# Kernel optimization log

Hardware: AMD Instinct MI355X
Metric: run time of the kernel (lower is better)

The kernel has to match this reference:

```python
import jax, jax.numpy as jnp
import numpy as np

TOPK = 300
NUM_LEVELS = 3
GATE_TEMP = 1.0


def _normalized_grid(h, w):
    # matches torch: linspace(-1,1) meshgrid 'ij', stack (xx, yy) -> [h*w, 2]
    y = jnp.linspace(-1.0, 1.0, h, dtype=jnp.float32)
    x = jnp.linspace(-1.0, 1.0, w, dtype=jnp.float32)
    yy, xx = jnp.meshgrid(y, x, indexing='ij')
    return jnp.stack((xx, yy), axis=-1).reshape(h * w, 2)


def setup_inputs() -> dict:
    key = jax.random.key(0)
    ks = jax.random.split(key, 10)
    C, H_DIM, MAXL = 256, 256, 8
    shapes = [(8, C, 100, 152), (8, C, 50, 76), (8, C, 25, 38)]
    inp = {}
    for i, s in enumerate(shapes):
        inp[f'f{i}'] = jax.random.normal(ks[i], s, dtype=jnp.float32)
    inp['conv_w'] = jax.random.normal(ks[3], (C,), dtype=jnp.float32) * (1.0 / np.sqrt(C))
    inp['conv_b'] = jnp.zeros((1,), dtype=jnp.float32)
    inp['level_emb'] = jax.random.normal(ks[4], (MAXL, H_DIM), dtype=jnp.float32)
    qin = C + H_DIM + 3  # 515
    inp['w1'] = jax.random.normal(ks[5], (qin, H_DIM), dtype=jnp.float32) * (1.0 / np.sqrt(qin))
    inp['b1'] = jnp.zeros((H_DIM,), dtype=jnp.float32)
    inp['w2'] = jax.random.normal(ks[6], (H_DIM, H_DIM), dtype=jnp.float32) * (1.0 / np.sqrt(H_DIM))
    inp['b2'] = jnp.zeros((H_DIM,), dtype=jnp.float32)
    inp['gate_w'] = jax.random.normal(ks[7], (H_DIM, MAXL), dtype=jnp.float32) * (1.0 / np.sqrt(H_DIM))
    inp['gate_b'] = jnp.zeros((MAXL,), dtype=jnp.float32)
    inp['residual_scale'] = jnp.zeros((1,), dtype=jnp.float32)  # residual_scale_init=0.0
    return inp


def reference(f0, f1, f2, conv_w, conv_b, level_emb, w1, b1, w2, b2, gate_w, gate_b, residual_scale):
    levels = [f0, f1, f2]
    B = f0.shape[0]
    tok_s, tok_f, tok_p, tok_l = [], [], [], []
    for i, f in enumerate(levels):
        _, C, H, W = f.shape
        # 1x1 conv proxy objectness score -> [B, H*W]
        s = jnp.einsum('bchw,c->bhw', f, conv_w).reshape(B, H * W) + conv_b[0]
        tok_s.append(s)
        tok_f.append(f.reshape(B, C, H * W).transpose(0, 2, 1))       # [B, HW, C]
        tok_p.append(jnp.broadcast_to(_normalized_grid(H, W), (B, H * W, 2)))
        tok_l.append(jnp.full((B, H * W), i, dtype=jnp.int32))
    scores = jnp.concatenate(tok_s, axis=1)   # [B, N]
    feats = jnp.concatenate(tok_f, axis=1)    # [B, N, C]
    pos = jnp.concatenate(tok_p, axis=1)      # [B, N, 2]
    lvl = jnp.concatenate(tok_l, axis=1)      # [B, N]

    top_vals, top_idx = jax.lax.top_k(scores, TOPK)                     # [B, K]
    fk = jnp.take_along_axis(feats, top_idx[:, :, None], axis=1)        # [B, K, C]
    pk = jnp.take_along_axis(pos, top_idx[:, :, None], axis=1)          # [B, K, 2]
    lk = jnp.take_along_axis(lvl, top_idx, axis=1)                      # [B, K]
    sp = jax.nn.sigmoid(top_vals)                                       # [B, K]

    q = jnp.concatenate([fk, level_emb[lk], pk, sp[..., None]], axis=-1)  # [B, K, C+H+3]
    h = jax.nn.relu(q @ w1 + b1)
    h = jax.nn.relu(h @ w2 + b2)
    logits = (h @ gate_w + gate_b)[..., :NUM_LEVELS]                     # [B, K, L]
    gates = jax.nn.softmax(logits / GATE_TEMP, axis=-1)
    alpha = gates.mean(axis=1)                                           # [B, L]
    scale = 1.0 + residual_scale[0] * alpha                              # [B, L]

    outs = [f * scale[:, i][:, None, None, None] for i, f in enumerate(levels)]
    # flatten the output feature dict into one [B, sum(C*H*W)] array
    return jnp.concatenate([o.reshape(B, -1) for o in outs], axis=1)
```

## Files before the change

kernel.cpp:

```cpp
#include <hip/hip_runtime.h>
#include <hip/hip_bf16.h>

#define NTOK 19950
#define NTOKP 19968
#define KTOP 300
#define NB 8
#define NQ 2400
#define QDIM 520
#define NCC 16

typedef float f32x4 __attribute__((ext_vector_type(4)));

__device__ __forceinline__ uint32_t fkey(float f) {
    uint32_t u = __float_as_uint(f);
    return (u & 0x80000000u) ? ~u : (u | 0x80000000u);
}

__global__ __launch_bounds__(256) void score_part_kernel(
    const float* __restrict__ f0, const float* __restrict__ f1, const float* __restrict__ f2,
    const float* __restrict__ conv_w, float* __restrict__ partial, int* __restrict__ ghist)
{
    __shared__ float cwch[16];
    const int tid = threadIdx.x;
    const int blk = blockIdx.x;
    int b, cc;
    if (blk < 512)      { b = blk >> 6; cc = (blk >> 2) & 15; }
    else if (blk < 640) { int i = blk - 512; b = i >> 4; cc = i & 15; }
    else                { int i = blk - 640; b = i >> 4; cc = i & 15; }
    if (blk >= 640 && ((blk - 640) & 15) == 0 && tid < 256)
        ghist[((blk - 640) >> 4) * 256 + tid] = 0;
    if (tid < 16) cwch[tid] = conv_w[cc * 16 + tid];
    __syncthreads();

    if (blk < 512) {
        const int q = blk & 3;
        const f32x4* b4 = (const f32x4*)(f0 + ((size_t)(b * 256 + cc * 16)) * 15200) + q * 950;
        const int s3 = (tid + 768 < 950) ? tid + 768 : 0;
        f32x4 a0 = {0,0,0,0}, a1 = a0, a2 = a0, a3 = a0;
        #pragma unroll 4
        for (int c = 0; c < 16; ++c) {
            const f32x4* r = b4 + (size_t)c * 3800;
            const float w = cwch[c];
            f32x4 v0 = r[tid], v1 = r[tid + 256], v2 = r[tid + 512], v3 = r[s3];
            a0 += v0 * w; a1 += v1 * w; a2 += v2 * w; a3 += v3 * w;
        }
        f32x4* o4 = (f32x4*)(partial + (size_t)(cc * NB + b) * NTOKP) + q * 950;
        o4[tid] = a0; o4[tid + 256] = a1; o4[tid + 512] = a2;
        if (tid + 768 < 950) o4[tid + 768] = a3;
    } else if (blk < 640) {
        const f32x4* b4 = (const f32x4*)(f1 + ((size_t)(b * 256 + cc * 16)) * 3800);
        const int s3 = (tid + 768 < 950) ? tid + 768 : 0;
        f32x4 a0 = {0,0,0,0}, a1 = a0, a2 = a0, a3 = a0;
        #pragma unroll 4
        for (int c = 0; c < 16; ++c) {
            const f32x4* r = b4 + (size_t)c * 950;
            const float w = cwch[c];
            f32x4 v0 = r[tid], v1 = r[tid + 256], v2 = r[tid + 512], v3 = r[s3];
            a0 += v0 * w; a1 += v1 * w; a2 += v2 * w; a3 += v3 * w;
        }
        f32x4* o4 = (f32x4*)(partial + (size_t)(cc * NB + b) * NTOKP + 15200);
        o4[tid] = a0; o4[tid + 256] = a1; o4[tid + 512] = a2;
        if (tid + 768 < 950) o4[tid + 768] = a3;
    } else {
        const float2* b2 = (const float2*)(f2 + ((size_t)(b * 256 + cc * 16)) * 950);
        const int s1 = (tid + 256 < 475) ? tid + 256 : 0;
        float2 a0 = {0,0}, a1 = a0;
        #pragma unroll 4
        for (int c = 0; c < 16; ++c) {
            const float2* r = b2 + (size_t)c * 475;
            const float w = cwch[c];
            float2 v0 = r[tid], v1 = r[s1];
            a0.x += v0.x * w; a0.y += v0.y * w;
            a1.x += v1.x * w; a1.y += v1.y * w;
        }
        float2* o2 = (float2*)(partial + (size_t)(cc * NB + b) * NTOKP + 19000);
        o2[tid] = a0;
        if (tid + 256 < 475) o2[tid + 256] = a1;
    }
}

__global__ __launch_bounds__(256) void score_reduce_kernel(
    const float* __restrict__ partial, const float* __restrict__ conv_b,
    float* __restrict__ scores, int* __restrict__ ghist)
{
    __shared__ int lh[256];
    const int tid = threadIdx.x;
    const int b = blockIdx.y;
    const int i = blockIdx.x * 256 + tid;
    lh[tid] = 0;
    __syncthreads();
    if (i < NTOK) {
        float s = 0.0f;
        #pragma unroll
        for (int cc = 0; cc < NCC; ++cc)
            s += partial[(size_t)(cc * NB + b) * NTOKP + i];
        s += conv_b[0];
        scores[b * NTOK + i] = s;
        atomicAdd(&lh[fkey(s) >> 24], 1);
    }
    __syncthreads();
    if (lh[tid]) atomicAdd(&ghist[b * 256 + tid], lh[tid]);
}

__global__ __launch_bounds__(1024, 1) void topk_kernel(
    const float* __restrict__ scores, const int* __restrict__ ghist,
    int* __restrict__ top_idx)
{
    __shared__ uint32_t key[NTOK];
    __shared__ int whist[16][256];
    __shared__ int suffix[257];
    __shared__ uint32_t s_prefix;
    __shared__ int s_Kr, s_cnt, s_tcnt;
    __shared__ int tie[1024];
    const int tid = threadIdx.x;
    const int wv = tid >> 6;
    const int b = blockIdx.x;
    const float* srow = scores + b * NTOK;
    for (int i = tid; i < NTOK; i += 1024) key[i] = fkey(srow[i]);
    if (tid == 0) { s_Kr = KTOP; suffix[256] = 0; }
    if (tid < 256) suffix[tid] = ghist[b * 256 + tid];
    __syncthreads();
    if (tid < 64) {
        const int c0 = suffix[tid * 4], c1 = suffix[tid * 4 + 1];
        const int c2 = suffix[tid * 4 + 2], c3 = suffix[tid * 4 + 3];
        const int tot = c0 + c1 + c2 + c3;
        int s = tot;
        #pragma unroll
        for (int off = 1; off < 64; off <<= 1) {
            int o = __shfl_down(s, off);
            if (tid + off < 64) s += o;
        }
        const int Sn = s - tot;
        suffix[tid * 4 + 3] = c3 + Sn;
        suffix[tid * 4 + 2] = c2 + c3 + Sn;
        suffix[tid * 4 + 1] = c1 + c2 + c3 + Sn;
        suffix[tid * 4 + 0] = tot + Sn;
    }
    __syncthreads();
    if (tid < 256) {
        int sgeq = suffix[tid];
        int sgt  = suffix[tid + 1];
        if (sgeq >= KTOP && sgt < KTOP) {
            s_prefix = (uint32_t)tid << 24;
            s_Kr = KTOP - sgt;
        }
    }
    __syncthreads();
    uint32_t pmask = 0xFF000000u;
    for (int pass = 1; pass < 4; ++pass) {
        const int shift = 24 - 8 * pass;
        for (int i = tid; i < 16 * 256; i += 1024) ((int*)whist)[i] = 0;
        __syncthreads();
        const uint32_t prefix = s_prefix;
        const int Kr = s_Kr;
        for (int i = tid; i < NTOK; i += 1024) {
            uint32_t k = key[i];
            if ((k & pmask) == prefix) atomicAdd(&whist[wv][(k >> shift) & 255], 1);
        }
        __syncthreads();
        if (tid < 256) {
            int s = 0;
            #pragma unroll
            for (int w = 0; w < 16; ++w) s += whist[w][tid];
            suffix[tid] = s;
        }
        __syncthreads();
        if (tid < 64) {
            const int c0 = suffix[tid * 4], c1 = suffix[tid * 4 + 1];
            const int c2 = suffix[tid * 4 + 2], c3 = suffix[tid * 4 + 3];
            const int tot = c0 + c1 + c2 + c3;
            int s = tot;
            #pragma unroll
            for (int off = 1; off < 64; off <<= 1) {
                int o = __shfl_down(s, off);
                if (tid + off < 64) s += o;
            }
            const int Sn = s - tot;
            suffix[tid * 4 + 3] = c3 + Sn;
            suffix[tid * 4 + 2] = c2 + c3 + Sn;
            suffix[tid * 4 + 1] = c1 + c2 + c3 + Sn;
            suffix[tid * 4 + 0] = tot + Sn;
        }
        __syncthreads();
        if (tid < 256) {
            int sgeq = suffix[tid];
            int sgt  = suffix[tid + 1];
            if (sgeq >= Kr && sgt < Kr) {
                s_prefix = prefix | ((uint32_t)tid << shift);
                s_Kr = Kr - sgt;
            }
        }
        __syncthreads();
        pmask |= (0xFFu << shift);
    }
    const uint32_t T = s_prefix;
    const int need = s_Kr;
    if (tid == 0) { s_cnt = 0; s_tcnt = 0; }
    __syncthreads();
    for (int i = tid; i < NTOK; i += 1024) {
        uint32_t k = key[i];
        if (k > T) {
            int p = atomicAdd(&s_cnt, 1);
            top_idx[b * KTOP + p] = i;
        } else if (k == T) {
            int p = atomicAdd(&s_tcnt, 1);
            if (p < 1024) tie[p] = i;
        }
    }
    __syncthreads();
    if (tid == 0) {
        int base = s_cnt;
        int tcnt = s_tcnt > 1024 ? 1024 : s_tcnt;
        for (int s = 0; s < need; ++s) {
            int mi = s;
            for (int u = s + 1; u < tcnt; ++u) if (tie[u] < tie[mi]) mi = u;
            int tmp = tie[s]; tie[s] = tie[mi]; tie[mi] = tmp;
            top_idx[b * KTOP + base + s] = tie[s];
        }
    }
}

#define QT 8
__global__ __launch_bounds__(512, 1) void mlp_kernel(
    const float* __restrict__ f0, const float* __restrict__ f1, const float* __restrict__ f2,
    const float* __restrict__ scores, const int* __restrict__ top_idx,
    const float* __restrict__ level_emb,
    const float* __restrict__ w1, const float* __restrict__ b1,
    const float* __restrict__ w2, const float* __restrict__ b2,
    const float* __restrict__ gate_w, const float* __restrict__ gate_b,
    float* __restrict__ G)
{
    __shared__ __align__(16) float q[QT][QDIM];
    __shared__ __align__(16) float part[QT][256];
    __shared__ __align__(16) float h[QT][256];
    __shared__ int s_b[QT], s_lvl[QT], s_hw[QT], s_HW[QT];
    const int tid = threadIdx.x;
    const int out = tid & 255;
    const int kh = tid >> 8;
    const int k0 = blockIdx.x * QT;

    if (tid < QT) {
        const int kk = k0 + tid;
        const int bq = kk / KTOP;
        const int idx = top_idx[kk];
        int lvl, hw, HWl, Wl, Hl;
        if (idx < 15200)      { lvl = 0; hw = idx;         HWl = 15200; Wl = 152; Hl = 100; }
        else if (idx < 19000) { lvl = 1; hw = idx - 15200; HWl = 3800;  Wl = 76;  Hl = 50;  }
        else                  { lvl = 2; hw = idx - 19000; HWl = 950;   Wl = 38;  Hl = 25;  }
        s_b[tid] = bq; s_lvl[tid] = lvl; s_hw[tid] = hw; s_HW[tid] = HWl;
        int hh = hw / Wl, ww = hw - hh * Wl;
        float x = -1.0f + 2.0f * (float)ww / (float)(Wl - 1);
        float y = -1.0f + 2.0f * (float)hh / (float)(Hl - 1);
        float sv = scores[bq * NTOK + idx];
        float sp = 1.0f / (1.0f + expf(-sv));
        q[tid][512] = x; q[tid][513] = y; q[tid][514] = sp;
        q[tid][515] = 0.0f; q[tid][516] = 0.0f; q[tid][517] = 0.0f;
        q[tid][518] = 0.0f; q[tid][519] = 0.0f;
    }
    __syncthreads();
    #pragma unroll
    for (int j = tid; j < QT * 256; j += 512) {
        const int t = j >> 8, c = j & 255;
        const int lvl = s_lvl[t];
        const float* f = (lvl == 0) ? f0 : ((lvl == 1) ? f1 : f2);
        q[t][c]       = f[((size_t)(s_b[t] * 256 + c)) * s_HW[t] + s_hw[t]];
        q[t][256 + c] = level_emb[lvl * 256 + c];
    }
    __syncthreads();

    float acc[QT];

    {
        #pragma unroll
        for (int t = 0; t < QT; ++t) acc[t] = 0.0f;
        const float* wp = w1 + (size_t)(kh * 256) * 256 + out;
        float a0 = wp[0], a1 = wp[256], a2 = wp[512], a3 = wp[768];
        for (int i4 = 0; i4 < 64; ++i4) {
            float c0 = a0, c1 = a1, c2 = a2, c3 = a3;
            const float* wn = wp + 1024;
            if (i4 < 63) { a0 = wn[0]; a1 = wn[256]; a2 = wn[512]; a3 = wn[768]; }
            wp = wn;
            const int kb = kh * 256 + i4 * 4;
            #pragma unroll
            for (int t = 0; t < QT; ++t) {
                float4 qv = *reinterpret_cast<const float4*>(&q[t][kb]);
                acc[t] += qv.x * c0 + qv.y * c1 + qv.z * c2 + qv.w * c3;
            }
        }
        if (kh) {
            for (int r = 512; r < 515; ++r) {
                float wv = w1[(size_t)r * 256 + out];
                #pragma unroll
                for (int t = 0; t < QT; ++t) acc[t] += q[t][r] * wv;
            }
            #pragma unroll
            for (int t = 0; t < QT; ++t) part[t][out] = acc[t];
        }
    }
    __syncthreads();
    if (kh == 0) {
        float bj = b1[out];
        #pragma unroll
        for (int t = 0; t < QT; ++t) h[t][out] = fmaxf(acc[t] + part[t][out] + bj, 0.0f);
    }
    __syncthreads();

    {
        #pragma unroll
        for (int t = 0; t < QT; ++t) acc[t] = 0.0f;
        const float* wp = w2 + (size_t)(kh * 128) * 256 + out;
        float a0 = wp[0], a1 = wp[256], a2 = wp[512], a3 = wp[768];
        for (int i4 = 0; i4 < 32; ++i4) {
            float c0 = a0, c1 = a1, c2 = a2, c3 = a3;
            const float* wn = wp + 1024;
            if (i4 < 31) { a0 = wn[0]; a1 = wn[256]; a2 = wn[512]; a3 = wn[768]; }
            wp = wn;
            const int kb = kh * 128 + i4 * 4;
            #pragma unroll
            for (int t = 0; t < QT; ++t) {
                float4 hv = *reinterpret_cast<const float4*>(&h[t][kb]);
                acc[t] += hv.x * c0 + hv.y * c1 + hv.z * c2 + hv.w * c3;
            }
        }
        if (kh) {
            #pragma unroll
            for (int t = 0; t < QT; ++t) part[t][out] = acc[t];
        }
    }
    __syncthreads();
    if (kh == 0) {
        float bj = b2[out];
        #pragma unroll
        for (int t = 0; t < QT; ++t) q[t][out] = fmaxf(acc[t] + part[t][out] + bj, 0.0f);
    }
    __syncthreads();

    if (tid < 256) {
        const int t = tid >> 5, seg = tid & 31;
        float l0 = 0.f, l1 = 0.f, l2 = 0.f;
        for (int c = seg * 8; c < seg * 8 + 8; ++c) {
            float hv = q[t][c];
            l0 += hv * gate_w[c * 8 + 0];
            l1 += hv * gate_w[c * 8 + 1];
            l2 += hv * gate_w[c * 8 + 2];
        }
        float* gp = &part[0][0];
        gp[(t * 32 + seg) * 3 + 0] = l0;
        gp[(t * 32 + seg) * 3 + 1] = l1;
        gp[(t * 32 + seg) * 3 + 2] = l2;
    }
    __syncthreads();
    if (tid < QT) {
        const int t = tid;
        float l0 = gate_b[0], l1 = gate_b[1], l2 = gate_b[2];
        const float* gp = &part[0][0];
        for (int seg = 0; seg < 32; ++seg) {
            l0 += gp[(t * 32 + seg) * 3 + 0];
            l1 += gp[(t * 32 + seg) * 3 + 1];
            l2 += gp[(t * 32 + seg) * 3 + 2];
        }
        float m = fmaxf(l0, fmaxf(l1, l2));
        float e0 = expf(l0 - m), e1 = expf(l1 - m), e2 = expf(l2 - m);
        float inv = 1.0f / (e0 + e1 + e2);
        G[(k0 + t) * 3 + 0] = e0 * inv;
        G[(k0 + t) * 3 + 1] = e1 * inv;
        G[(k0 + t) * 3 + 2] = e2 * inv;
    }
}

__global__ __launch_bounds__(256) void out_kernel(
    const f32x4* __restrict__ f0, const f32x4* __restrict__ f1, const f32x4* __restrict__ f2,
    const float* __restrict__ G, const float* __restrict__ rs, f32x4* __restrict__ out)
{
    __shared__ float red[3][32];
    __shared__ float ssc[3];
    const int b = blockIdx.y;
    const int tid = threadIdx.x;
    if (tid < 96) {
        const int l = tid / 32, c = tid % 32;
        float s = 0.0f;
        const int kb = c * 10;
        const int ke = (kb + 10 < KTOP) ? kb + 10 : KTOP;
        for (int k = kb; k < ke; ++k) s += G[(size_t)(b * KTOP + k) * 3 + l];
        red[l][c] = s;
    }
    __syncthreads();
    for (int off = 16; off > 0; off >>= 1) {
        if (tid < 96) {
            const int l = tid / 32, c = tid % 32;
            if (c < off) red[l][c] += red[l][c + off];
        }
        __syncthreads();
    }
    if (tid < 3) ssc[tid] = 1.0f + rs[0] * (red[tid][0] / (float)KTOP);
    __syncthreads();

    const int t0 = blockIdx.x * 256 + tid;
    const int TPB = gridDim.x * 256;
    f32x4* ob = out + (size_t)b * 1276800;
    {
        const float sc = ssc[0];
        const f32x4* src = f0 + (size_t)b * 972800;
        for (int r = t0; r < 972800; r += TPB)
            __builtin_nontemporal_store(src[r] * sc, &ob[r]);
    }
    {
        const float sc = ssc[1];
        const f32x4* src = f1 + (size_t)b * 243200;
        f32x4* o1 = ob + 972800;
        for (int r = t0; r < 243200; r += TPB)
            __builtin_nontemporal_store(src[r] * sc, &o1[r]);
    }
    {
        const float sc = ssc[2];
        const f32x4* src = f2 + (size_t)b * 60800;
        f32x4* o2 = ob + 1216000;
        for (int r = t0; r < 60800; r += TPB)
            __builtin_nontemporal_store(src[r] * sc, &o2[r]);
    }
}

extern "C" void kernel_launch(void* const* d_in, const int* in_sizes, int n_in,
                              void* d_out, int out_size, void* d_ws, size_t ws_size,
                              hipStream_t stream)
{
    const float* f0        = (const float*)d_in[0];
    const float* f1        = (const float*)d_in[1];
    const float* f2        = (const float*)d_in[2];
    const float* conv_w    = (const float*)d_in[3];
    const float* conv_b    = (const float*)d_in[4];
    const float* level_emb = (const float*)d_in[5];
    const float* w1        = (const float*)d_in[6];
    const float* b1        = (const float*)d_in[7];
    const float* w2        = (const float*)d_in[8];
    const float* b2        = (const float*)d_in[9];
    const float* gate_w    = (const float*)d_in[10];
    const float* gate_b    = (const float*)d_in[11];
    const float* rs        = (const float*)d_in[12];

    char* ws = (char*)d_ws;
    float* scores  = (float*)ws;
    int*   top_idx = (int*)(ws + 640 * 1024);
    float* G       = (float*)(ws + 656 * 1024);
    int*   ghist   = (int*)(ws + 688 * 1024);
    float* partial = (float*)(ws + 704 * 1024);

    score_part_kernel<<<768, 256, 0, stream>>>(f0, f1, f2, conv_w, partial, ghist);
    score_reduce_kernel<<<dim3(78, NB), 256, 0, stream>>>(partial, conv_b, scores, ghist);
    topk_kernel<<<NB, 1024, 0, stream>>>(scores, ghist, top_idx);
    mlp_kernel<<<NQ / QT, 512, 0, stream>>>(f0, f1, f2, scores, top_idx, level_emb,
                                            w1, b1, w2, b2, gate_w, gate_b, G);
    out_kernel<<<dim3(256, NB), 256, 0, stream>>>((const f32x4*)f0, (const f32x4*)f1,
                                                  (const f32x4*)f2, G, rs, (f32x4*)d_out);
}
```

Before: 150.2 us.

## Compact top-k candidates to top-byte bucket and widen output kernel grid

The top-k kernel no longer stores all 19950 keys in shared memory. It emits elements whose top byte lies above the threshold bucket directly and compacts the threshold-bucket elements into a small candidate buffer, so the three refinement passes scan only those candidates. It falls back to rescanning global scores when more than 4096 candidates land in the bucket. The per-wave histograms become a single shared histogram, which means more atomic contention but much less shared memory. The out_kernel grid is doubled from 256 to 512 blocks per batch, and a store guard is added in the score kernel.

```diff
diff --git a/kernel.cpp b/kernel.cpp
--- a/kernel.cpp
+++ b/kernel.cpp
@@ -8,12 +8,32 @@
 #define NQ 2400
 #define QDIM 520
 #define NCC 16
+#define CAND 4096
 
 typedef float f32x4 __attribute__((ext_vector_type(4)));
 
 __device__ __forceinline__ uint32_t fkey(float f) {
     uint32_t u = __float_as_uint(f);
     return (u & 0x80000000u) ? ~u : (u | 0x80000000u);
+}
+
+__device__ __forceinline__ void suffix_scan_256(int* hist, int tid) {
+    if (tid < 64) {
+        const int c0 = hist[tid * 4], c1 = hist[tid * 4 + 1];
+        const int c2 = hist[tid * 4 + 2], c3 = hist[tid * 4 + 3];
+        const int tot = c0 + c1 + c2 + c3;
+        int s = tot;
+        #pragma unroll
+        for (int off = 1; off < 64; off <<= 1) {
+            int o = __shfl_down(s, off);
+            if (tid + off < 64) s += o;
+        }
+        const int Sn = s - tot;
+        hist[tid * 4 + 3] = c3 + Sn;
+        hist[tid * 4 + 2] = c2 + c3 + Sn;
+        hist[tid * 4 + 1] = c1 + c2 + c3 + Sn;
+        hist[tid * 4 + 0] = tot + Sn;
+    }
 }
 
 __global__ __launch_bounds__(256) void score_part_kernel(
@@ -74,7 +94,7 @@
             a1.x += v1.x * w; a1.y += v1.y * w;
         }
         float2* o2 = (float2*)(partial + (size_t)(cc * NB + b) * NTOKP + 19000);
-        o2[tid] = a0;
+        if (tid < 475) o2[tid] = a0;
         if (tid + 256 < 475) o2[tid + 256] = a1;
     }
 }
@@ -106,85 +126,70 @@
     const float* __restrict__ scores, const int* __restrict__ ghist,
     int* __restrict__ top_idx)
 {
-    __shared__ uint32_t key[NTOK];
-    __shared__ int whist[16][256];
-    __shared__ int suffix[257];
+    __shared__ int hist[257];
+    __shared__ uint32_t ck[CAND];
+    __shared__ int ci[CAND];
+    __shared__ int tie[1024];
     __shared__ uint32_t s_prefix;
-    __shared__ int s_Kr, s_cnt, s_tcnt;
-    __shared__ int tie[1024];
+    __shared__ int s_Kr, s_cnt, s_ccnt, s_tcnt;
     const int tid = threadIdx.x;
-    const int wv = tid >> 6;
     const int b = blockIdx.x;
     const float* srow = scores + b * NTOK;
-    for (int i = tid; i < NTOK; i += 1024) key[i] = fkey(srow[i]);
-    if (tid == 0) { s_Kr = KTOP; suffix[256] = 0; }
-    if (tid < 256) suffix[tid] = ghist[b * 256 + tid];
-    __syncthreads();
-    if (tid < 64) {
-        const int c0 = suffix[tid * 4], c1 = suffix[tid * 4 + 1];
-        const int c2 = suffix[tid * 4 + 2], c3 = suffix[tid * 4 + 3];
-        const int tot = c0 + c1 + c2 + c3;
-        int s = tot;
-        #pragma unroll
-        for (int off = 1; off < 64; off <<= 1) {
-            int o = __shfl_down(s, off);
-            if (tid + off < 64) s += o;
-        }
-        const int Sn = s - tot;
-        suffix[tid * 4 + 3] = c3 + Sn;
-        suffix[tid * 4 + 2] = c2 + c3 + Sn;
-        suffix[tid * 4 + 1] = c1 + c2 + c3 + Sn;
-        suffix[tid * 4 + 0] = tot + Sn;
-    }
+
+    if (tid < 256) hist[tid] = ghist[b * 256 + tid];
+    if (tid == 0) { hist[256] = 0; s_cnt = 0; s_ccnt = 0; s_tcnt = 0; }
+    __syncthreads();
+    suffix_scan_256(hist, tid);
     __syncthreads();
     if (tid < 256) {
-        int sgeq = suffix[tid];
-        int sgt  = suffix[tid + 1];
+        int sgeq = hist[tid], sgt = hist[tid + 1];
         if (sgeq >= KTOP && sgt < KTOP) {
             s_prefix = (uint32_t)tid << 24;
             s_Kr = KTOP - sgt;
         }
     }
     __syncthreads();
+    const uint32_t v = s_prefix >> 24;
+
+    for (int i = tid; i < NTOK; i += 1024) {
+        uint32_t k = fkey(srow[i]);
+        uint32_t tb = k >> 24;
+        if (tb > v) {
+            int p = atomicAdd(&s_cnt, 1);
+            top_idx[b * KTOP + p] = i;
+        } else if (tb == v) {
+            int p = atomicAdd(&s_ccnt, 1);
+            if (p < CAND) { ck[p] = k; ci[p] = i; }
+        }
+    }
+    __syncthreads();
+    const int ccnt = s_ccnt;
+    const int ncand = ccnt < CAND ? ccnt : CAND;
+    const bool fits = (ccnt <= CAND);
+
     uint32_t pmask = 0xFF000000u;
     for (int pass = 1; pass < 4; ++pass) {
         const int shift = 24 - 8 * pass;
-        for (int i = tid; i < 16 * 256; i += 1024) ((int*)whist)[i] = 0;
+        if (tid < 257) hist[tid] = 0;
         __syncthreads();
         const uint32_t prefix = s_prefix;
         const int Kr = s_Kr;
-        for (int i = tid; i < NTOK; i += 1024) {
-            uint32_t k = key[i];
-            if ((k & pmask) == prefix) atomicAdd(&whist[wv][(k >> shift) & 255], 1);
-        }
+        if (fits) {
+            for (int j = tid; j < ncand; j += 1024) {
+                uint32_t k = ck[j];
+                if ((k & pmask) == prefix) atomicAdd(&hist[(k >> shift) & 255], 1);
+            }
+        } else {
+            for (int i = tid; i < NTOK; i += 1024) {
+                uint32_t k = fkey(srow[i]);
+                if ((k & pmask) == prefix) atomicAdd(&hist[(k >> shift) & 255], 1);
+            }
+        }
+        __syncthreads();
+        suffix_scan_256(hist, tid);
         __syncthreads();
         if (tid < 256) {
-            int s = 0;
-            #pragma unroll
-            for (int w = 0; w < 16; ++w) s += whist[w][tid];
-            suffix[tid] = s;
-        }
-        __syncthreads();
-        if (tid < 64) {
-            const int c0 = suffix[tid * 4], c1 = suffix[tid * 4 + 1];
-            const int c2 = suffix[tid * 4 + 2], c3 = suffix[tid * 4 + 3];
-            const int tot = c0 + c1 + c2 + c3;
-            int s = tot;
-            #pragma unroll
-            for (int off = 1; off < 64; off <<= 1) {
-                int o = __shfl_down(s, off);
-                if (tid + off < 64) s += o;
-            }
-            const int Sn = s - tot;
-            suffix[tid * 4 + 3] = c3 + Sn;
-            suffix[tid * 4 + 2] = c2 + c3 + Sn;
-            suffix[tid * 4 + 1] = c1 + c2 + c3 + Sn;
-            suffix[tid * 4 + 0] = tot + Sn;
-        }
-        __syncthreads();
-        if (tid < 256) {
-            int sgeq = suffix[tid];
-            int sgt  = suffix[tid + 1];
+            int sgeq = hist[tid], sgt = hist[tid + 1];
             if (sgeq >= Kr && sgt < Kr) {
                 s_prefix = prefix | ((uint32_t)tid << shift);
                 s_Kr = Kr - sgt;
@@ -195,16 +200,30 @@
     }
     const uint32_t T = s_prefix;
     const int need = s_Kr;
-    if (tid == 0) { s_cnt = 0; s_tcnt = 0; }
-    __syncthreads();
-    for (int i = tid; i < NTOK; i += 1024) {
-        uint32_t k = key[i];
-        if (k > T) {
-            int p = atomicAdd(&s_cnt, 1);
-            top_idx[b * KTOP + p] = i;
-        } else if (k == T) {
-            int p = atomicAdd(&s_tcnt, 1);
-            if (p < 1024) tie[p] = i;
+
+    if (fits) {
+        for (int j = tid; j < ncand; j += 1024) {
+            uint32_t k = ck[j];
+            if (k > T) {
+                int p = atomicAdd(&s_cnt, 1);
+                top_idx[b * KTOP + p] = ci[j];
+            } else if (k == T) {
+                int p = atomicAdd(&s_tcnt, 1);
+                if (p < 1024) tie[p] = ci[j];
+            }
+        }
+    } else {
+        for (int i = tid; i < NTOK; i += 1024) {
+            uint32_t k = fkey(srow[i]);
+            if ((k >> 24) == v) {
+                if (k > T) {
+                    int p = atomicAdd(&s_cnt, 1);
+                    top_idx[b * KTOP + p] = i;
+                } else if (k == T) {
+                    int p = atomicAdd(&s_tcnt, 1);
+                    if (p < 1024) tie[p] = i;
+                }
+            }
         }
     }
     __syncthreads();
@@ -450,6 +469,6 @@
     topk_kernel<<<NB, 1024, 0, stream>>>(scores, ghist, top_idx);
     mlp_kernel<<<NQ / QT, 512, 0, stream>>>(f0, f1, f2, scores, top_idx, level_emb,
                                             w1, b1, w2, b2, gate_w, gate_b, G);
-    out_kernel<<<dim3(256, NB), 256, 0, stream>>>((const f32x4*)f0, (const f32x4*)f1,
+    out_kernel<<<dim3(512, NB), 256, 0, stream>>>((const f32x4*)f0, (const f32x4*)f1,
                                                   (const f32x4*)f2, G, rs, (f32x4*)d_out);
 }
```

New measurement: 164.8 us. 9.7% more time.
